# Kernel optimization log

Measured on AMD Instinct MI355X. Metric: run time of the kernel, lower is better.

Reference implementation:

```python
import jax, jax.numpy as jnp
import numpy as np

B, T, D = 2, 2048, 1024
NH = 16
HD = D // NH


def setup_inputs() -> dict:
    key = jax.random.key(0)
    ks = jax.random.split(key, 5)
    s = 0.02
    return {
        "x": jax.random.normal(ks[0], (B, T, D), dtype=jnp.float32),
        "Wq": jax.random.normal(ks[1], (D, D), dtype=jnp.float32) * s,
        "Wk": jax.random.normal(ks[2], (D, D), dtype=jnp.float32) * s,
        "Wv": jax.random.normal(ks[3], (D, D), dtype=jnp.float32) * s,
        "Wo": jax.random.normal(ks[4], (D, D), dtype=jnp.float32) * s,
        "bo": jnp.zeros((D,), dtype=jnp.float32),
    }


def reference(x, Wq, Wk, Wv, Wo, bo):
    b, t, _ = x.shape
    scale = HD ** -0.5
    # torch Linear: y = x @ W^T
    q = (x @ Wq.T).reshape(b, t, NH, HD)
    k = (x @ Wk.T).reshape(b, t, NH, HD)
    v = (x @ Wv.T).reshape(b, t, NH, HD)
    # scores: [b, nh, t, t]
    s = jnp.einsum("bqhd,bkhd->bhqk", q, k) * scale
    causal = jnp.tril(jnp.ones((t, t), dtype=bool))
    s = jnp.where(causal, s, -jnp.inf)
    p = jax.nn.softmax(s, axis=-1)
    o = jnp.einsum("bhqk,bkhd->bqhd", p, v).reshape(b, t, D)
    return o @ Wo.T + bo
```

## Files before the change

### kernel.cpp

```cpp
#include <hip/hip_runtime.h>


typedef __bf16 bf16x8 __attribute__((ext_vector_type(8)));
typedef float f32x4 __attribute__((ext_vector_type(4)));
typedef unsigned short ushortx8 __attribute__((ext_vector_type(8)));
typedef unsigned short ushortx4 __attribute__((ext_vector_type(4)));

#define T_SEQ 2048
#define NHEAD 16
#define HDIM 64
#define DMODEL 1024

__device__ inline unsigned short f2bf(float f) {
  unsigned int u = __builtin_bit_cast(unsigned int, f);
  unsigned int r = (u + 0x7fffu + ((u >> 16) & 1u)) >> 16;
  return (unsigned short)r;
}

__device__ inline void gl16(const unsigned short* g, unsigned short* l) {
  __builtin_amdgcn_global_load_lds(
      (const __attribute__((address_space(1))) unsigned int*)g,
      (__attribute__((address_space(3))) unsigned int*)l, 16, 0, 0);
}

__global__ void cast_all(const float* __restrict__ x, const float* __restrict__ w0,
                         const float* __restrict__ w1, const float* __restrict__ w2,
                         const float* __restrict__ w3, unsigned short* __restrict__ out) {
  const int NX = 2 * T_SEQ * DMODEL;
  int i = (blockIdx.x * 256 + threadIdx.x) * 4;
  const float* src;
  int off;
  if (i < NX) {
    src = x; off = i;
  } else {
    const int j = i - NX;
    const int sel = j >> 20;
    off = j & ((1 << 20) - 1);
    src = sel == 0 ? w0 : sel == 1 ? w1 : sel == 2 ? w2 : w3;
  }
  float4 v = *reinterpret_cast<const float4*>(src + off);
  ushortx4 o;
  o[0] = f2bf(v.x); o[1] = f2bf(v.y); o[2] = f2bf(v.z); o[3] = f2bf(v.w);
  *reinterpret_cast<ushortx4*>(out + i) = o;
}

__device__ __forceinline__ void gemm_core(
    const unsigned short* __restrict__ A, const unsigned short* __restrict__ Bw,
    int K, int m0, int n0, f32x4 acc[4][4]) {
  __shared__ unsigned short As[4096];
  __shared__ unsigned short Bs[4096];
  const int tid = threadIdx.x;
  const int lane = tid & 63, wid = tid >> 6;
  const int wr = wid >> 1, wc = wid & 1;
  const int lr = lane & 15, lg = lane >> 4;
  const int srow = tid >> 2;
  const int scs = ((tid & 3) ^ (srow & 3)) * 8;
  const unsigned short* ga0 = A + (size_t)(m0 + srow) * K + scs;
  const unsigned short* gb0 = Bw + (size_t)(n0 + srow) * K + scs;
  unsigned short* la0 = As + tid * 8;
  unsigned short* lb0 = Bs + tid * 8;
  const int rca = (lg ^ (lr & 3)) * 8;

  for (int k0 = 0; k0 < K; k0 += 32) {
    __syncthreads();
    gl16(ga0 + k0, la0);
    gl16(ga0 + (size_t)64 * K + k0, la0 + 2048);
    gl16(gb0 + k0, lb0);
    gl16(gb0 + (size_t)64 * K + k0, lb0 + 2048);
    __syncthreads();

    bf16x8 af[4], bfr[4];
#pragma unroll
    for (int t = 0; t < 4; ++t) {
      af[t]  = *reinterpret_cast<const bf16x8*>(&As[(wr * 64 + t * 16 + lr) * 32 + rca]);
      bfr[t] = *reinterpret_cast<const bf16x8*>(&Bs[(wc * 64 + t * 16 + lr) * 32 + rca]);
    }
#pragma unroll
    for (int mi = 0; mi < 4; ++mi)
#pragma unroll
      for (int ni = 0; ni < 4; ++ni)
        acc[mi][ni] = __builtin_amdgcn_mfma_f32_16x16x32_bf16(af[mi], bfr[ni], acc[mi][ni], 0, 0, 0);
  }
}

__device__ __forceinline__ void gemm_core_n64(
    const unsigned short* __restrict__ A, const unsigned short* __restrict__ Bw,
    int K, int m0, int n0, f32x4 acc[4][2]) {
  __shared__ unsigned short As[4096];
  __shared__ unsigned short Bs[2048];
  const int tid = threadIdx.x;
  const int lane = tid & 63, wid = tid >> 6;
  const int wr = wid >> 1, wc = wid & 1;
  const int lr = lane & 15, lg = lane >> 4;
  const int srow = tid >> 2;
  const int scs = ((tid & 3) ^ (srow & 3)) * 8;
  const unsigned short* ga0 = A + (size_t)(m0 + srow) * K + scs;
  const unsigned short* gb0 = Bw + (size_t)(n0 + srow) * K + scs;
  unsigned short* la0 = As + tid * 8;
  unsigned short* lb0 = Bs + tid * 8;
  const int rca = (lg ^ (lr & 3)) * 8;

  for (int k0 = 0; k0 < K; k0 += 32) {
    __syncthreads();
    gl16(ga0 + k0, la0);
    gl16(ga0 + (size_t)64 * K + k0, la0 + 2048);
    gl16(gb0 + k0, lb0);
    __syncthreads();

    bf16x8 af[4], bfr[2];
#pragma unroll
    for (int t = 0; t < 4; ++t)
      af[t] = *reinterpret_cast<const bf16x8*>(&As[(wr * 64 + t * 16 + lr) * 32 + rca]);
#pragma unroll
    for (int t = 0; t < 2; ++t)
      bfr[t] = *reinterpret_cast<const bf16x8*>(&Bs[(wc * 32 + t * 16 + lr) * 32 + rca]);
#pragma unroll
    for (int mi = 0; mi < 4; ++mi)
#pragma unroll
      for (int ni = 0; ni < 2; ++ni)
        acc[mi][ni] = __builtin_amdgcn_mfma_f32_16x16x32_bf16(af[mi], bfr[ni], acc[mi][ni], 0, 0, 0);
  }
}

__global__ __launch_bounds__(256) void gemm_qkv(
    const unsigned short* __restrict__ xb, const unsigned short* __restrict__ Wall,
    unsigned short* __restrict__ Qb, unsigned short* __restrict__ Kb,
    unsigned short* __restrict__ Vtb) {
  const int z = blockIdx.y;
  const int bid = blockIdx.x;
  int m0, n0;
  const unsigned short* A;
  const unsigned short* Bw;
  if (z < 2) {
    n0 = (bid & 7) * 128; m0 = (bid >> 3) * 128;
    A = xb; Bw = Wall + (size_t)z * (DMODEL * DMODEL);
  } else {
    m0 = (bid & 7) * 128; n0 = (bid >> 3) * 128;
    A = Wall + (size_t)2 * (DMODEL * DMODEL); Bw = xb;
  }
  f32x4 acc[4][4] = {};
  gemm_core(A, Bw, DMODEL, m0, n0, acc);

  const int tid = threadIdx.x, lane = tid & 63, wid = tid >> 6;
  const int wr = wid >> 1, wc = wid & 1, lr = lane & 15, lg = lane >> 4;
  const int mb = m0 + wr * 64, nb = n0 + wc * 64;
  const float scale = z == 0 ? 0.125f * 1.44269504089f : 1.0f;
#pragma unroll
  for (int mi = 0; mi < 4; ++mi)
#pragma unroll
    for (int ni = 0; ni < 4; ++ni) {
      const int col = nb + ni * 16 + lr;
#pragma unroll
      for (int j = 0; j < 4; ++j) {
        const int row = mb + mi * 16 + lg * 4 + j;
        const float v = acc[mi][ni][j] * scale;
        if (z < 2) {
          const int b = row >> 11, t = row & (T_SEQ - 1);
          const int h = col >> 6, d = col & (HDIM - 1);
          unsigned short* out = z == 0 ? Qb : Kb;
          out[(((size_t)(b * NHEAD + h) * T_SEQ + t) << 6) + d] = f2bf(v);
        } else {
          const int h = row >> 6, d = row & (HDIM - 1);
          const int b = col >> 11, tt = col & (T_SEQ - 1);
          const int nib = (tt >> 2) & 7;
          const int nib2 = ((nib & 3) << 1) | (nib >> 2);
          const int tp = (tt & ~31) | (nib2 << 2) | (tt & 3);
          Vtb[(((size_t)(b * NHEAD + h) * HDIM + d) << 11) + tp] = f2bf(v);
        }
      }
    }
}

__global__ __launch_bounds__(256) void gemm_proj(
    const unsigned short* __restrict__ Ob, const unsigned short* __restrict__ Wob,
    float* __restrict__ out, const float* __restrict__ bias) {
  const int m0 = blockIdx.y * 128, n0 = blockIdx.x * 64;
  f32x4 acc[4][2] = {};
  gemm_core_n64(Ob, Wob, DMODEL, m0, n0, acc);

  const int tid = threadIdx.x, lane = tid & 63, wid = tid >> 6;
  const int wr = wid >> 1, wc = wid & 1, lr = lane & 15, lg = lane >> 4;
  const int mb = m0 + wr * 64, nb = n0 + wc * 32;
#pragma unroll
  for (int mi = 0; mi < 4; ++mi)
#pragma unroll
    for (int ni = 0; ni < 2; ++ni) {
      const int col = nb + ni * 16 + lr;
      const float bv = bias[col];
#pragma unroll
      for (int j = 0; j < 4; ++j) {
        const int row = mb + mi * 16 + lg * 4 + j;
        out[(size_t)row * DMODEL + col] = acc[mi][ni][j] + bv;
      }
    }
}

__device__ __forceinline__ void attn_step(
    const unsigned short* Kslot, const unsigned short* Vslot,
    const int kh0, const int kh1, const int (&vo)[2],
    const bf16x8 (&qf)[2], f32x4 (&acc)[4], float& lrun,
    const bool domask, const int kb, const int q, const int lg) {
  f32x4 s[4] = {};
  __builtin_amdgcn_s_setprio(1);
#pragma unroll
  for (int c = 0; c < 4; ++c) {
    bf16x8 k0 = *reinterpret_cast<const bf16x8*>(&Kslot[kh0 + c * 1024]);
    bf16x8 k1 = *reinterpret_cast<const bf16x8*>(&Kslot[kh1 + c * 1024]);
    s[c] = __builtin_amdgcn_mfma_f32_16x16x32_bf16(k0, qf[0], s[c], 0, 0, 0);
    s[c] = __builtin_amdgcn_mfma_f32_16x16x32_bf16(k1, qf[1], s[c], 0, 0, 0);
  }
  __builtin_amdgcn_s_setprio(0);
  if (domask) {
#pragma unroll
    for (int c = 0; c < 4; ++c)
#pragma unroll
      for (int j = 0; j < 4; ++j) {
        const int k = kb + c * 16 + lg * 4 + j;
        if (k > q) s[c][j] = -INFINITY;
      }
  }
  float tsum = 0.f;
#pragma unroll
  for (int c = 0; c < 4; ++c)
#pragma unroll
    for (int j = 0; j < 4; ++j) {
      const float p = exp2f(s[c][j]);
      s[c][j] = p;
      tsum += p;
    }
  lrun += tsum;

  bf16x8 pb[2];
#pragma unroll
  for (int ks = 0; ks < 2; ++ks) {
    bf16x8 t8;
#pragma unroll
    for (int e = 0; e < 8; ++e) t8[e] = (__bf16)s[ks * 2 + (e >> 2)][e & 3];
    pb[ks] = t8;
  }
  __builtin_amdgcn_s_setprio(1);
#pragma unroll
  for (int dt = 0; dt < 4; ++dt)
#pragma unroll
    for (int ks = 0; ks < 2; ++ks) {
      bf16x8 vf = *reinterpret_cast<const bf16x8*>(&Vslot[vo[ks] + dt * 1024]);
      acc[dt] = __builtin_amdgcn_mfma_f32_16x16x32_bf16(vf, pb[ks], acc[dt], 0, 0, 0);
    }
  __builtin_amdgcn_s_setprio(0);
}

__global__ __launch_bounds__(512, 4) void flash_attn(
    const unsigned short* __restrict__ Q, const unsigned short* __restrict__ Kg,
    const unsigned short* __restrict__ Vt, unsigned short* __restrict__ O) {
  __shared__ unsigned short Ks[5][4096];
  __shared__ unsigned short Vs[5][4096];
  const int tid = threadIdx.x, lane = tid & 63, wid = tid >> 6;
  const int lr = lane & 15, lg = lane >> 4, wq = wid & 3;
  const int bid = blockIdx.x;
  const int bh = (bid & 7) * 4 + ((bid >> 3) & 3);
  const int a = (bid >> 5) & 15;
  const int b = 31 - a;
  const bool g0 = wid < 4;
  const int myq1 = g0 ? a : b;
  const int q1 = myq1 * 64 + wq * 16 + lr;
  const int q2 = b * 64 + wq * 16 + lr;
  const size_t base = (size_t)bh * (T_SEQ * HDIM);

  bf16x8 qf1[2], qf2[2];
#pragma unroll
  for (int h = 0; h < 2; ++h) {
    qf1[h] = *reinterpret_cast<const bf16x8*>(Q + base + (size_t)q1 * HDIM + h * 32 + lg * 8);
    qf2[h] = *reinterpret_cast<const bf16x8*>(Q + base + (size_t)q2 * HDIM + h * 32 + lg * 8);
  }

  const int srow = tid >> 3;
  const int schk = ((tid & 7) ^ (srow & 7)) * 8;
  const unsigned short* kst = Kg + base + (size_t)srow * HDIM + schk;
  const unsigned short* vst = Vt + base + (size_t)srow * T_SEQ + schk;

#define STAGE(slot, kt_)                                \
  do {                                                  \
    const int kb_ = (kt_) * 64;                         \
    gl16(kst + (size_t)kb_ * HDIM, &Ks[slot][tid * 8]); \
    gl16(vst + kb_, &Vs[slot][tid * 8]);                \
  } while (0)

  const int kh0 = lr * 64 + ((lg ^ (lr & 7)) * 8);
  const int kh1 = lr * 64 + (((4 + lg) ^ (lr & 7)) * 8);
  int vo[2];
#pragma unroll
  for (int ks = 0; ks < 2; ++ks)
    vo[ks] = lr * 64 + (((ks * 4 + lg) ^ (lr & 7)) * 8);

  float l1 = 0.f, l2 = 0.f;
  f32x4 acc1[4] = {}, acc2[4] = {};

  STAGE(0, 0);
  STAGE(1, 1);
  asm volatile("s_waitcnt vmcnt(2)" ::: "memory");
  __builtin_amdgcn_s_barrier();
  asm volatile("" ::: "memory");

  int sl = 0;
  for (int kt = 0; kt <= a; ++kt) {
    const int st = kt + 2;
    int sst = sl + 2; if (sst >= 5) sst -= 5;
    if (st <= b) STAGE(sst, st);
    attn_step(Ks[sl], Vs[sl], kh0, kh1, vo, qf1, acc1, l1,
              g0 && (kt == a), kt * 64, q1, lg);
    if (kt < a && st <= b) {
      asm volatile("s_waitcnt vmcnt(2)" ::: "memory");
    } else {
      asm volatile("s_waitcnt vmcnt(0)" ::: "memory");
    }
    __builtin_amdgcn_s_barrier();
    asm volatile("" ::: "memory");
    ++sl; if (sl >= 5) sl -= 5;
  }

  {
    int s3 = sl + 2; if (s3 >= 5) s3 -= 5;
    if (a + 3 <= b) STAGE(s3, a + 3);
  }
  for (int t0 = a + 1; t0 <= b; t0 += 2) {
    int s1 = sl + 1; if (s1 >= 5) s1 -= 5;
    int s3 = sl + 3; if (s3 >= 5) s3 -= 5;
    int s4 = sl + 4; if (s4 >= 5) s4 -= 5;
    if (t0 + 3 <= b) STAGE(s3, t0 + 3);
    if (t0 + 4 <= b) STAGE(s4, t0 + 4);
    if (!g0) {
      attn_step(Ks[sl], Vs[sl], kh0, kh1, vo, qf2, acc1, l1,
                t0 == b, t0 * 64, q2, lg);
    } else if (t0 + 1 <= b) {
      attn_step(Ks[s1], Vs[s1], kh0, kh1, vo, qf2, acc2, l2,
                false, (t0 + 1) * 64, q2, lg);
    }
    if (t0 + 4 <= b) {
      asm volatile("s_waitcnt vmcnt(2)" ::: "memory");
    } else {
      asm volatile("s_waitcnt vmcnt(0)" ::: "memory");
    }
    __builtin_amdgcn_s_barrier();
    asm volatile("" ::: "memory");
    sl += 2; if (sl >= 5) sl -= 5;
  }
#undef STAGE

  float* sm = reinterpret_cast<float*>(&Ks[0][0]);
  const int lid = (wq * 64 + lane) * 18;
  if (g0) {
    float* p = sm + lid;
    p[0] = l2;
#pragma unroll
    for (int dt = 0; dt < 4; ++dt)
#pragma unroll
      for (int j = 0; j < 4; ++j) p[2 + dt * 4 + j] = acc2[dt][j];
  }
  __syncthreads();
  if (!g0) {
    const float* p = sm + lid;
    l1 += p[0];
#pragma unroll
    for (int dt = 0; dt < 4; ++dt)
#pragma unroll
      for (int j = 0; j < 4; ++j)
        acc1[dt][j] += p[2 + dt * 4 + j];
  }

  l1 += __shfl_xor(l1, 16, 64);
  l1 += __shfl_xor(l1, 32, 64);

  const int b_ = bh >> 4, h_ = bh & (NHEAD - 1);
  const float inv = 1.0f / l1;
  unsigned short* orow = O + (((size_t)(b_ * T_SEQ + q1)) << 10) + h_ * HDIM + lg * 4;
#pragma unroll
  for (int dt = 0; dt < 4; ++dt) {
    ushortx4 o4;
#pragma unroll
    for (int j = 0; j < 4; ++j) o4[j] = f2bf(acc1[dt][j] * inv);
    *reinterpret_cast<ushortx4*>(orow + dt * 16) = o4;
  }
}

extern "C" void kernel_launch(void* const* d_in, const int* in_sizes, int n_in,
                              void* d_out, int out_size, void* d_ws, size_t ws_size,
                              hipStream_t stream) {
  const float* x  = (const float*)d_in[0];
  const float* Wq = (const float*)d_in[1];
  const float* Wk = (const float*)d_in[2];
  const float* Wv = (const float*)d_in[3];
  const float* Wo = (const float*)d_in[4];
  const float* bo = (const float*)d_in[5];
  float* out = (float*)d_out;

  const int M = 2 * T_SEQ;
  const int NXD = DMODEL * DMODEL;
  const int NX = M * DMODEL;

  unsigned short* ws = (unsigned short*)d_ws;
  unsigned short* xb  = ws;
  unsigned short* Wqb = xb + NX;
  unsigned short* Wob = Wqb + 3 * (size_t)NXD;
  unsigned short* Qb  = Wqb + 4 * (size_t)NXD;
  unsigned short* Kbf = Qb + NX;
  unsigned short* Vtb = Kbf + NX;
  unsigned short* Ob  = Vtb + NX;

  cast_all<<<(NX + 4 * NXD) / 1024, 256, 0, stream>>>(x, Wq, Wk, Wv, Wo, xb);

  dim3 gq(256, 3);
  gemm_qkv<<<gq, 256, 0, stream>>>(xb, Wqb, Qb, Kbf, Vtb);

  flash_attn<<<512, 512, 0, stream>>>(Qb, Kbf, Vtb, Ob);

  dim3 gg(DMODEL / 64, M / 128);
  gemm_proj<<<gg, 256, 0, stream>>>(Ob, Wob, out, bo);
}
```

Measured before the change: 100.2 us.

## Double GEMM K-tile, restructure attention loop, compute softmax row sums via MFMA

The GEMM cores now stage a 64-wide K slice per iteration with 8-way XOR swizzle, halving the number of barrier-synchronised iterations at the cost of double the LDS footprint. The attention kernel merges its two phases into one loop that processes two KV tiles per barrier, and stages three tiles up front. Softmax denominators are accumulated with an extra pair of MFMAs against a ones vector instead of scalar adds and cross-lane shuffles, which also makes the sum use bf16-rounded probabilities, consistent with the PV product.

Result: slower. 108.5 us (+8.2%).

```diff
diff --git a/kernel.cpp b/kernel.cpp
--- a/kernel.cpp
+++ b/kernel.cpp
@@ -47,78 +47,84 @@
 __device__ __forceinline__ void gemm_core(
     const unsigned short* __restrict__ A, const unsigned short* __restrict__ Bw,
     int K, int m0, int n0, f32x4 acc[4][4]) {
-  __shared__ unsigned short As[4096];
+  __shared__ unsigned short As[8192];
+  __shared__ unsigned short Bs[8192];
+  const int tid = threadIdx.x;
+  const int lane = tid & 63, wid = tid >> 6;
+  const int wr = wid >> 1, wc = wid & 1;
+  const int lr = lane & 15, lg = lane >> 4;
+  const int srow = tid >> 3;
+  const int schk = ((tid & 7) ^ (srow & 7)) * 8;
+  const unsigned short* ga0 = A + (size_t)(m0 + srow) * K + schk;
+  const unsigned short* gb0 = Bw + (size_t)(n0 + srow) * K + schk;
+  const int rc[2] = { ((lg) ^ (lr & 7)) * 8, ((4 + lg) ^ (lr & 7)) * 8 };
+
+  for (int k0 = 0; k0 < K; k0 += 64) {
+    __syncthreads();
+#pragma unroll
+    for (int i = 0; i < 4; ++i) {
+      gl16(ga0 + (size_t)(i * 32) * K + k0, &As[i * 2048 + tid * 8]);
+      gl16(gb0 + (size_t)(i * 32) * K + k0, &Bs[i * 2048 + tid * 8]);
+    }
+    __syncthreads();
+
+#pragma unroll
+    for (int ks = 0; ks < 2; ++ks) {
+      bf16x8 af[4], bfr[4];
+#pragma unroll
+      for (int t = 0; t < 4; ++t) {
+        af[t]  = *reinterpret_cast<const bf16x8*>(&As[(wr * 64 + t * 16 + lr) * 64 + rc[ks]]);
+        bfr[t] = *reinterpret_cast<const bf16x8*>(&Bs[(wc * 64 + t * 16 + lr) * 64 + rc[ks]]);
+      }
+#pragma unroll
+      for (int mi = 0; mi < 4; ++mi)
+#pragma unroll
+        for (int ni = 0; ni < 4; ++ni)
+          acc[mi][ni] = __builtin_amdgcn_mfma_f32_16x16x32_bf16(af[mi], bfr[ni], acc[mi][ni], 0, 0, 0);
+    }
+  }
+}
+
+__device__ __forceinline__ void gemm_core_n64(
+    const unsigned short* __restrict__ A, const unsigned short* __restrict__ Bw,
+    int K, int m0, int n0, f32x4 acc[4][2]) {
+  __shared__ unsigned short As[8192];
   __shared__ unsigned short Bs[4096];
   const int tid = threadIdx.x;
   const int lane = tid & 63, wid = tid >> 6;
   const int wr = wid >> 1, wc = wid & 1;
   const int lr = lane & 15, lg = lane >> 4;
-  const int srow = tid >> 2;
-  const int scs = ((tid & 3) ^ (srow & 3)) * 8;
-  const unsigned short* ga0 = A + (size_t)(m0 + srow) * K + scs;
-  const unsigned short* gb0 = Bw + (size_t)(n0 + srow) * K + scs;
-  unsigned short* la0 = As + tid * 8;
-  unsigned short* lb0 = Bs + tid * 8;
-  const int rca = (lg ^ (lr & 3)) * 8;
-
-  for (int k0 = 0; k0 < K; k0 += 32) {
+  const int srow = tid >> 3;
+  const int schk = ((tid & 7) ^ (srow & 7)) * 8;
+  const unsigned short* ga0 = A + (size_t)(m0 + srow) * K + schk;
+  const unsigned short* gb0 = Bw + (size_t)(n0 + srow) * K + schk;
+  const int rc[2] = { ((lg) ^ (lr & 7)) * 8, ((4 + lg) ^ (lr & 7)) * 8 };
+
+  for (int k0 = 0; k0 < K; k0 += 64) {
     __syncthreads();
-    gl16(ga0 + k0, la0);
-    gl16(ga0 + (size_t)64 * K + k0, la0 + 2048);
-    gl16(gb0 + k0, lb0);
-    gl16(gb0 + (size_t)64 * K + k0, lb0 + 2048);
+#pragma unroll
+    for (int i = 0; i < 4; ++i)
+      gl16(ga0 + (size_t)(i * 32) * K + k0, &As[i * 2048 + tid * 8]);
+#pragma unroll
+    for (int i = 0; i < 2; ++i)
+      gl16(gb0 + (size_t)(i * 32) * K + k0, &Bs[i * 2048 + tid * 8]);
     __syncthreads();
 
-    bf16x8 af[4], bfr[4];
-#pragma unroll
-    for (int t = 0; t < 4; ++t) {
-      af[t]  = *reinterpret_cast<const bf16x8*>(&As[(wr * 64 + t * 16 + lr) * 32 + rca]);
-      bfr[t] = *reinterpret_cast<const bf16x8*>(&Bs[(wc * 64 + t * 16 + lr) * 32 + rca]);
-    }
-#pragma unroll
-    for (int mi = 0; mi < 4; ++mi)
-#pragma unroll
-      for (int ni = 0; ni < 4; ++ni)
-        acc[mi][ni] = __builtin_amdgcn_mfma_f32_16x16x32_bf16(af[mi], bfr[ni], acc[mi][ni], 0, 0, 0);
-  }
-}
-
-__device__ __forceinline__ void gemm_core_n64(
-    const unsigned short* __restrict__ A, const unsigned short* __restrict__ Bw,
-    int K, int m0, int n0, f32x4 acc[4][2]) {
-  __shared__ unsigned short As[4096];
-  __shared__ unsigned short Bs[2048];
-  const int tid = threadIdx.x;
-  const int lane = tid & 63, wid = tid >> 6;
-  const int wr = wid >> 1, wc = wid & 1;
-  const int lr = lane & 15, lg = lane >> 4;
-  const int srow = tid >> 2;
-  const int scs = ((tid & 3) ^ (srow & 3)) * 8;
-  const unsigned short* ga0 = A + (size_t)(m0 + srow) * K + scs;
-  const unsigned short* gb0 = Bw + (size_t)(n0 + srow) * K + scs;
-  unsigned short* la0 = As + tid * 8;
-  unsigned short* lb0 = Bs + tid * 8;
-  const int rca = (lg ^ (lr & 3)) * 8;
-
-  for (int k0 = 0; k0 < K; k0 += 32) {
-    __syncthreads();
-    gl16(ga0 + k0, la0);
-    gl16(ga0 + (size_t)64 * K + k0, la0 + 2048);
-    gl16(gb0 + k0, lb0);
-    __syncthreads();
-
-    bf16x8 af[4], bfr[2];
-#pragma unroll
-    for (int t = 0; t < 4; ++t)
-      af[t] = *reinterpret_cast<const bf16x8*>(&As[(wr * 64 + t * 16 + lr) * 32 + rca]);
-#pragma unroll
-    for (int t = 0; t < 2; ++t)
-      bfr[t] = *reinterpret_cast<const bf16x8*>(&Bs[(wc * 32 + t * 16 + lr) * 32 + rca]);
-#pragma unroll
-    for (int mi = 0; mi < 4; ++mi)
-#pragma unroll
-      for (int ni = 0; ni < 2; ++ni)
-        acc[mi][ni] = __builtin_amdgcn_mfma_f32_16x16x32_bf16(af[mi], bfr[ni], acc[mi][ni], 0, 0, 0);
+#pragma unroll
+    for (int ks = 0; ks < 2; ++ks) {
+      bf16x8 af[4], bfr[2];
+#pragma unroll
+      for (int t = 0; t < 4; ++t)
+        af[t] = *reinterpret_cast<const bf16x8*>(&As[(wr * 64 + t * 16 + lr) * 64 + rc[ks]]);
+#pragma unroll
+      for (int t = 0; t < 2; ++t)
+        bfr[t] = *reinterpret_cast<const bf16x8*>(&Bs[(wc * 32 + t * 16 + lr) * 64 + rc[ks]]);
+#pragma unroll
+      for (int mi = 0; mi < 4; ++mi)
+#pragma unroll
+        for (int ni = 0; ni < 2; ++ni)
+          acc[mi][ni] = __builtin_amdgcn_mfma_f32_16x16x32_bf16(af[mi], bfr[ni], acc[mi][ni], 0, 0, 0);
+    }
   }
 }
 
@@ -195,10 +201,24 @@
     }
 }
 
+__device__ __forceinline__ void sm_pack(f32x4 (&s)[4], bf16x8 (&pb)[2]) {
+#pragma unroll
+  for (int c = 0; c < 4; ++c)
+#pragma unroll
+    for (int j = 0; j < 4; ++j) s[c][j] = exp2f(s[c][j]);
+#pragma unroll
+  for (int ks = 0; ks < 2; ++ks) {
+    bf16x8 t8;
+#pragma unroll
+    for (int e = 0; e < 8; ++e) t8[e] = (__bf16)s[ks * 2 + (e >> 2)][e & 3];
+    pb[ks] = t8;
+  }
+}
+
 __device__ __forceinline__ void attn_step(
     const unsigned short* Kslot, const unsigned short* Vslot,
     const int kh0, const int kh1, const int (&vo)[2],
-    const bf16x8 (&qf)[2], f32x4 (&acc)[4], float& lrun,
+    const bf16x8 (&qf)[2], f32x4 (&acc)[4], f32x4& lacc, const bf16x8 ones,
     const bool domask, const int kb, const int q, const int lg) {
   f32x4 s[4] = {};
   __builtin_amdgcn_s_setprio(1);
@@ -219,25 +239,8 @@
         if (k > q) s[c][j] = -INFINITY;
       }
   }
-  float tsum = 0.f;
-#pragma unroll
-  for (int c = 0; c < 4; ++c)
-#pragma unroll
-    for (int j = 0; j < 4; ++j) {
-      const float p = exp2f(s[c][j]);
-      s[c][j] = p;
-      tsum += p;
-    }
-  lrun += tsum;
-
   bf16x8 pb[2];
-#pragma unroll
-  for (int ks = 0; ks < 2; ++ks) {
-    bf16x8 t8;
-#pragma unroll
-    for (int e = 0; e < 8; ++e) t8[e] = (__bf16)s[ks * 2 + (e >> 2)][e & 3];
-    pb[ks] = t8;
-  }
+  sm_pack(s, pb);
   __builtin_amdgcn_s_setprio(1);
 #pragma unroll
   for (int dt = 0; dt < 4; ++dt)
@@ -246,6 +249,8 @@
       bf16x8 vf = *reinterpret_cast<const bf16x8*>(&Vslot[vo[ks] + dt * 1024]);
       acc[dt] = __builtin_amdgcn_mfma_f32_16x16x32_bf16(vf, pb[ks], acc[dt], 0, 0, 0);
     }
+  lacc = __builtin_amdgcn_mfma_f32_16x16x32_bf16(ones, pb[0], lacc, 0, 0, 0);
+  lacc = __builtin_amdgcn_mfma_f32_16x16x32_bf16(ones, pb[1], lacc, 0, 0, 0);
   __builtin_amdgcn_s_setprio(0);
 }
 
@@ -272,6 +277,9 @@
     qf1[h] = *reinterpret_cast<const bf16x8*>(Q + base + (size_t)q1 * HDIM + h * 32 + lg * 8);
     qf2[h] = *reinterpret_cast<const bf16x8*>(Q + base + (size_t)q2 * HDIM + h * 32 + lg * 8);
   }
+  bf16x8 ones;
+#pragma unroll
+  for (int e = 0; e < 8; ++e) ones[e] = (__bf16)1.0f;
 
   const int srow = tid >> 3;
   const int schk = ((tid & 7) ^ (srow & 7)) * 8;
@@ -292,49 +300,48 @@
   for (int ks = 0; ks < 2; ++ks)
     vo[ks] = lr * 64 + (((ks * 4 + lg) ^ (lr & 7)) * 8);
 
-  float l1 = 0.f, l2 = 0.f;
   f32x4 acc1[4] = {}, acc2[4] = {};
+  f32x4 lacc1 = {}, lacc2 = {};
 
   STAGE(0, 0);
   STAGE(1, 1);
+  STAGE(2, 2);
   asm volatile("s_waitcnt vmcnt(2)" ::: "memory");
   __builtin_amdgcn_s_barrier();
   asm volatile("" ::: "memory");
 
   int sl = 0;
-  for (int kt = 0; kt <= a; ++kt) {
-    const int st = kt + 2;
-    int sst = sl + 2; if (sst >= 5) sst -= 5;
-    if (st <= b) STAGE(sst, st);
-    attn_step(Ks[sl], Vs[sl], kh0, kh1, vo, qf1, acc1, l1,
-              g0 && (kt == a), kt * 64, q1, lg);
-    if (kt < a && st <= b) {
-      asm volatile("s_waitcnt vmcnt(2)" ::: "memory");
-    } else {
-      asm volatile("s_waitcnt vmcnt(0)" ::: "memory");
-    }
-    __builtin_amdgcn_s_barrier();
-    asm volatile("" ::: "memory");
-    ++sl; if (sl >= 5) sl -= 5;
-  }
-
-  {
-    int s3 = sl + 2; if (s3 >= 5) s3 -= 5;
-    if (a + 3 <= b) STAGE(s3, a + 3);
-  }
-  for (int t0 = a + 1; t0 <= b; t0 += 2) {
+  for (int t0 = 0; t0 <= b; t0 += 2) {
     int s1 = sl + 1; if (s1 >= 5) s1 -= 5;
     int s3 = sl + 3; if (s3 >= 5) s3 -= 5;
     int s4 = sl + 4; if (s4 >= 5) s4 -= 5;
     if (t0 + 3 <= b) STAGE(s3, t0 + 3);
     if (t0 + 4 <= b) STAGE(s4, t0 + 4);
-    if (!g0) {
-      attn_step(Ks[sl], Vs[sl], kh0, kh1, vo, qf2, acc1, l1,
+
+    if (t0 <= a) {
+      attn_step(Ks[sl], Vs[sl], kh0, kh1, vo, qf1, acc1, lacc1, ones,
+                g0 && (t0 == a), t0 * 64, q1, lg);
+    } else if (((t0 - a) & 1) && !g0) {
+      attn_step(Ks[sl], Vs[sl], kh0, kh1, vo, qf2, acc1, lacc1, ones,
                 t0 == b, t0 * 64, q2, lg);
-    } else if (t0 + 1 <= b) {
-      attn_step(Ks[s1], Vs[s1], kh0, kh1, vo, qf2, acc2, l2,
-                false, (t0 + 1) * 64, q2, lg);
-    }
+    } else if (!((t0 - a) & 1) && g0) {
+      attn_step(Ks[sl], Vs[sl], kh0, kh1, vo, qf2, acc2, lacc2, ones,
+                false, t0 * 64, q2, lg);
+    }
+    const int t1 = t0 + 1;
+    if (t1 <= b) {
+      if (t1 <= a) {
+        attn_step(Ks[s1], Vs[s1], kh0, kh1, vo, qf1, acc1, lacc1, ones,
+                  g0 && (t1 == a), t1 * 64, q1, lg);
+      } else if (((t1 - a) & 1) && !g0) {
+        attn_step(Ks[s1], Vs[s1], kh0, kh1, vo, qf2, acc1, lacc1, ones,
+                  t1 == b, t1 * 64, q2, lg);
+      } else if (!((t1 - a) & 1) && g0) {
+        attn_step(Ks[s1], Vs[s1], kh0, kh1, vo, qf2, acc2, lacc2, ones,
+                  false, t1 * 64, q2, lg);
+      }
+    }
+
     if (t0 + 4 <= b) {
       asm volatile("s_waitcnt vmcnt(2)" ::: "memory");
     } else {
@@ -350,13 +357,14 @@
   const int lid = (wq * 64 + lane) * 18;
   if (g0) {
     float* p = sm + lid;
-    p[0] = l2;
+    p[0] = lacc2[0];
 #pragma unroll
     for (int dt = 0; dt < 4; ++dt)
 #pragma unroll
       for (int j = 0; j < 4; ++j) p[2 + dt * 4 + j] = acc2[dt][j];
   }
   __syncthreads();
+  float l1 = lacc1[0];
   if (!g0) {
     const float* p = sm + lid;
     l1 += p[0];
@@ -366,9 +374,6 @@
       for (int j = 0; j < 4; ++j)
         acc1[dt][j] += p[2 + dt * 4 + j];
   }
-
-  l1 += __shfl_xor(l1, 16, 64);
-  l1 += __shfl_xor(l1, 32, 64);
 
   const int b_ = bh >> 4, h_ = bh & (NHEAD - 1);
   const float inv = 1.0f / l1;
```
